# Kernel tuning notes

Hardware: AMD Instinct MI355X
Metric: run time of the kernel (lower is better)

Reference implementation:

```python
import jax, jax.numpy as jnp
import numpy as np

N_NODES = 50000


def _gcn_conv(x, edge_index, W, b):
    """PyG-style GCNConv: add self-loops, symmetric deg^-1/2 norm, linear + scatter-add + bias."""
    n = x.shape[0]
    # add self loops
    loop = jnp.arange(n, dtype=edge_index.dtype)
    src = jnp.concatenate([edge_index[0], loop])  # [E+N]
    dst = jnp.concatenate([edge_index[1], loop])
    ones = jnp.ones_like(dst, dtype=x.dtype)
    deg = jax.ops.segment_sum(ones, dst, num_segments=n)  # in-degree incl. self loop
    deg_inv_sqrt = jnp.where(deg > 0, jax.lax.rsqrt(deg), 0.0)
    norm = deg_inv_sqrt[src] * deg_inv_sqrt[dst]  # [E+N]
    h = x @ W  # [N, out]
    msg = h[src] * norm[:, None]  # gather + scale, [E+N, out]
    out = jax.ops.segment_sum(msg, dst, num_segments=n)  # scatter-add
    return out + b


def setup_inputs() -> dict:
    key = jax.random.key(0)
    k1, k2, k3, k4 = jax.random.split(key, 4)
    in_ch, hid, z = 128, 128, 64
    x = jax.random.normal(k1, (N_NODES, in_ch), dtype=jnp.float32)
    edge_index = jax.random.randint(k2, (2, 800000), 0, N_NODES, dtype=jnp.int64)
    W1 = jax.random.normal(k3, (in_ch, hid), dtype=jnp.float32) * (1.0 / np.sqrt(in_ch))
    b1 = jnp.zeros((hid,), dtype=jnp.float32)
    W2 = jax.random.normal(k4, (hid, z), dtype=jnp.float32) * (1.0 / np.sqrt(hid))
    b2 = jnp.zeros((z,), dtype=jnp.float32)
    return {"x": x, "edge_index": edge_index, "W1": W1, "b1": b1, "W2": W2, "b2": b2}


def reference(x, edge_index, W1, b1, W2, b2):
    h = jax.nn.relu(_gcn_conv(x, edge_index, W1, b1))
    return _gcn_conv(h, edge_index, W2, b2)
```

## Files before the change

kernel.cpp:

```cpp
#include <hip/hip_runtime.h>

static constexpr int K = 128;

using ushort8 = __attribute__((ext_vector_type(8))) unsigned short;
using bf16x8  = __attribute__((ext_vector_type(8))) __bf16;
using f32x4   = __attribute__((ext_vector_type(4))) float;

__device__ inline float bflo(unsigned u) { return __uint_as_float(u << 16); }
__device__ inline float bfhi(unsigned u) { return __uint_as_float(u & 0xFFFF0000u); }
__device__ inline unsigned short f2bf(float f) {
    unsigned u = __float_as_uint(f);
    return (unsigned short)((u + 0x7FFF + ((u >> 16) & 1)) >> 16);
}


__global__ __launch_bounds__(256) void k_zerob(int* __restrict__ bcnt) {
    bcnt[threadIdx.x] = 0;
}

__global__ __launch_bounds__(256) void k_bcount(const int* __restrict__ dst, int e,
                                                int* __restrict__ bcnt, int nb) {
    __shared__ int c[256];
    int t = threadIdx.x;
    c[t] = 0;
    __syncthreads();
    for (int i = blockIdx.x * 256 + t; i < e; i += gridDim.x * 256)
        atomicAdd(&c[dst[i] >> 8], 1);
    __syncthreads();
    if (t < nb && c[t]) atomicAdd(&bcnt[t], c[t]);
}

__global__ __launch_bounds__(256) void k_bscan(const int* __restrict__ bcnt,
                                               int* __restrict__ bbase,
                                               int* __restrict__ gcur,
                                               int nb, int* __restrict__ offs,
                                               int n, int e) {
    __shared__ int sh[256];
    int t = threadIdx.x;
    int v = (t < nb) ? bcnt[t] : 0;
    sh[t] = v;
    __syncthreads();
    for (int o = 1; o < 256; o <<= 1) {
        int x = (t >= o) ? sh[t - o] : 0;
        __syncthreads();
        sh[t] += x;
        __syncthreads();
    }
    int excl = sh[t] - v;
    bbase[t] = excl;
    gcur[t] = excl;
    if (t == 255) bbase[256] = sh[255];
    if (t == 0) offs[n] = e;
}

__global__ __launch_bounds__(256) void k_bin(const int* __restrict__ ei, int e,
                                             int* __restrict__ gcur,
                                             unsigned long long* __restrict__ tmp) {
    constexpr int PER = 8;
    __shared__ int cnt[256], base[256], cur[256];
    int t = threadIdx.x;
    int chunk0 = blockIdx.x * 256 * PER;
    cnt[t] = 0;
    __syncthreads();
    int ds[PER];
#pragma unroll
    for (int k2 = 0; k2 < PER; ++k2) {
        int i = chunk0 + k2 * 256 + t;
        ds[k2] = (i < e) ? ei[(size_t)e + i] : -1;
        if (ds[k2] >= 0) atomicAdd(&cnt[ds[k2] >> 8], 1);
    }
    __syncthreads();
    int c = cnt[t];
    base[t] = c ? atomicAdd(&gcur[t], c) : 0;
    cur[t] = 0;
    __syncthreads();
#pragma unroll
    for (int k2 = 0; k2 < PER; ++k2) {
        int i = chunk0 + k2 * 256 + t;
        if (i < e) {
            int b = ds[k2] >> 8;
            int pos = base[b] + atomicAdd(&cur[b], 1);
            tmp[pos] = ((unsigned long long)(unsigned)ds[k2] << 32) | (unsigned)ei[i];
        }
    }
}

__global__ __launch_bounds__(256) void k_csr(const unsigned long long* __restrict__ tmp,
                                             const int* __restrict__ bbase,
                                             int* __restrict__ offs,
                                             int* __restrict__ srt,
                                             float* __restrict__ dinv, int n) {
    __shared__ int cntS[256], sh[256], cur[256];
    int b = blockIdx.x;
    int t = threadIdx.x;
    int beg = bbase[b], end = bbase[b + 1];
    cntS[t] = 0;
    __syncthreads();
    for (int i = beg + t; i < end; i += 256)
        atomicAdd(&cntS[(int)(tmp[i] >> 32) & 255], 1);
    __syncthreads();
    int v = cntS[t];
    sh[t] = v;
    __syncthreads();
    for (int o = 1; o < 256; o <<= 1) {
        int x = (t >= o) ? sh[t - o] : 0;
        __syncthreads();
        sh[t] += x;
        __syncthreads();
    }
    int pfx = sh[t] - v;
    int node = b * 256 + t;
    if (node < n) {
        offs[node] = beg + pfx;
        dinv[node] = rsqrtf((float)(v + 1));
    }
    cur[t] = pfx;
    __syncthreads();
    for (int i = beg + t; i < end; i += 256) {
        unsigned long long pr = tmp[i];
        int d = (int)(pr >> 32);
        int pos = atomicAdd(&cur[d & 255], 1);
        srt[beg + pos] = (int)(pr & 0xFFFFFFFFu);
    }
}


template <int COUT>
__global__ __launch_bounds__(256) void k_gemm_mfma(const float* __restrict__ X,
                                                   const float* __restrict__ W,
                                                   const float* __restrict__ dinv,
                                                   unsigned short* __restrict__ G, int n) {
    constexpr int BM = 64, BK = 32;
    constexpr int NCT = COUT / 16;
    constexpr int NCH = K / BK;
    constexpr int WT = COUT * (BK / 8) / 256;
    __shared__ unsigned short Ah[BM * BK], Al[BM * BK];
    __shared__ unsigned short Bh[COUT * BK], Bl[COUT * BK];
    __shared__ float dS[BM];
    const int tid = threadIdx.x;
    const int row0 = blockIdx.x * BM;
    if (tid < BM) {
        int gr = row0 + tid;
        dS[tid] = (gr < n) ? dinv[gr] : 0.f;
    }

    float4 xr[2];
    float wr[WT][8];

    auto loadX = [&](int kc) {
        int r = tid >> 2, ks = tid & 3;
        int gr = row0 + r;
        if (gr < n) {
            const float4* pp = (const float4*)(X + (size_t)gr * K + kc * BK + ks * 8);
            xr[0] = pp[0];
            xr[1] = pp[1];
        } else {
            xr[0] = make_float4(0.f, 0.f, 0.f, 0.f);
            xr[1] = xr[0];
        }
    };
    auto loadW = [&](int kc) {
#pragma unroll
        for (int q = 0; q < WT; ++q) {
            int i = tid + q * 256;
            int c = i % COUT, ks = i / COUT;
#pragma unroll
            for (int j = 0; j < 8; ++j)
                wr[q][j] = W[(size_t)(kc * BK + ks * 8 + j) * COUT + c];
        }
    };
    auto storeLDS = [&]() {
        int r = tid >> 2, ks = tid & 3;
        ushort8 h, l;
        const float* f = (const float*)&xr[0];
#pragma unroll
        for (int j = 0; j < 8; ++j) {
            unsigned short hh = f2bf(f[j]);
            h[j] = hh;
            l[j] = f2bf(f[j] - __uint_as_float((unsigned)hh << 16));
        }
        *(ushort8*)&Ah[r * BK + ks * 8] = h;
        *(ushort8*)&Al[r * BK + ks * 8] = l;
#pragma unroll
        for (int q = 0; q < WT; ++q) {
            int i = tid + q * 256;
            int c = i % COUT, ks2 = i / COUT;
            ushort8 wh, wl;
#pragma unroll
            for (int j = 0; j < 8; ++j) {
                unsigned short hh = f2bf(wr[q][j]);
                wh[j] = hh;
                wl[j] = f2bf(wr[q][j] - __uint_as_float((unsigned)hh << 16));
            }
            *(ushort8*)&Bh[c * BK + ks2 * 8] = wh;
            *(ushort8*)&Bl[c * BK + ks2 * 8] = wl;
        }
    };

    f32x4 acc[NCT] = {};
    const int l = tid & 63, wv = tid >> 6;
    const int l16 = l & 15, lk = l >> 4;
    const int arow = wv * 16 + l16;

    loadX(0);
    loadW(0);
    storeLDS();
    __syncthreads();
    for (int c = 0; c < NCH; ++c) {
        if (c + 1 < NCH) { loadX(c + 1); loadW(c + 1); }
        bf16x8 ah = *(const bf16x8*)&Ah[arow * BK + lk * 8];
        bf16x8 al = *(const bf16x8*)&Al[arow * BK + lk * 8];
#pragma unroll
        for (int ct = 0; ct < NCT; ++ct) {
            bf16x8 bh = *(const bf16x8*)&Bh[(ct * 16 + l16) * BK + lk * 8];
            bf16x8 bl = *(const bf16x8*)&Bl[(ct * 16 + l16) * BK + lk * 8];
            acc[ct] = __builtin_amdgcn_mfma_f32_16x16x32_bf16(ah, bh, acc[ct], 0, 0, 0);
            acc[ct] = __builtin_amdgcn_mfma_f32_16x16x32_bf16(al, bh, acc[ct], 0, 0, 0);
            acc[ct] = __builtin_amdgcn_mfma_f32_16x16x32_bf16(ah, bl, acc[ct], 0, 0, 0);
        }
        if (c + 1 < NCH) {
            __syncthreads();
            storeLDS();
            __syncthreads();
        }
    }

#pragma unroll
    for (int ct = 0; ct < NCT; ++ct) {
        int col = ct * 16 + l16;
#pragma unroll
        for (int r4 = 0; r4 < 4; ++r4) {
            int lr = wv * 16 + lk * 4 + r4;
            int gr = row0 + lr;
            if (gr < n) G[(size_t)gr * COUT + col] = f2bf(acc[ct][r4] * dS[lr]);
        }
    }
}


#define ADD8(u)                                      \
    do {                                             \
        a[0] += bflo((u).x); a[1] += bfhi((u).x);    \
        a[2] += bflo((u).y); a[3] += bfhi((u).y);    \
        a[4] += bflo((u).z); a[5] += bfhi((u).z);    \
        a[6] += bflo((u).w); a[7] += bfhi((u).w);    \
    } while (0)

template <bool RELU>
__global__ __launch_bounds__(256) void k_reduce128(const int* __restrict__ offs,
                                                   const int* __restrict__ srt,
                                                   const uint4* __restrict__ g4,
                                                   const float* __restrict__ dinv,
                                                   const float* __restrict__ bias,
                                                   float* __restrict__ out, int n) {
    int node = blockIdx.x * 4 + (threadIdx.x >> 6);
    if (node >= n) return;
    int lane = threadIdx.x & 63;
    int l16 = lane & 15, grp = lane >> 4;
    int beg = offs[node], end = offs[node + 1];

    float a[8] = {};
    if (grp == 0) {
        uint4 u = g4[(size_t)node * 16 + l16];
        ADD8(u);
    }
    int j = beg + grp;
    for (; j + 12 < end; j += 16) {
        uint4 u0 = g4[(size_t)srt[j]      * 16 + l16];
        uint4 u1 = g4[(size_t)srt[j + 4]  * 16 + l16];
        uint4 u2 = g4[(size_t)srt[j + 8]  * 16 + l16];
        uint4 u3 = g4[(size_t)srt[j + 12] * 16 + l16];
        ADD8(u0); ADD8(u1); ADD8(u2); ADD8(u3);
    }
    for (; j < end; j += 4) {
        uint4 u = g4[(size_t)srt[j] * 16 + l16];
        ADD8(u);
    }
#pragma unroll
    for (int q = 0; q < 8; ++q) {
        a[q] += __shfl_xor(a[q], 16);
        a[q] += __shfl_xor(a[q], 32);
    }
    if (lane < 16) {
        float di = dinv[node];
        float4 b0 = ((const float4*)bias)[l16 * 2];
        float4 b1 = ((const float4*)bias)[l16 * 2 + 1];
        float4 o0, o1;
        o0.x = fmaf(di, a[0], b0.x); o0.y = fmaf(di, a[1], b0.y);
        o0.z = fmaf(di, a[2], b0.z); o0.w = fmaf(di, a[3], b0.w);
        o1.x = fmaf(di, a[4], b1.x); o1.y = fmaf(di, a[5], b1.y);
        o1.z = fmaf(di, a[6], b1.z); o1.w = fmaf(di, a[7], b1.w);
        if (RELU) {
            o0.x = fmaxf(o0.x, 0.f); o0.y = fmaxf(o0.y, 0.f);
            o0.z = fmaxf(o0.z, 0.f); o0.w = fmaxf(o0.w, 0.f);
            o1.x = fmaxf(o1.x, 0.f); o1.y = fmaxf(o1.y, 0.f);
            o1.z = fmaxf(o1.z, 0.f); o1.w = fmaxf(o1.w, 0.f);
        }
        float4* op = (float4*)(out + (size_t)node * 128 + l16 * 8);
        op[0] = o0;
        op[1] = o1;
    }
}

template <bool RELU>
__global__ __launch_bounds__(256) void k_reduce64(const int* __restrict__ offs,
                                                  const int* __restrict__ srt,
                                                  const uint4* __restrict__ g4,
                                                  const float* __restrict__ dinv,
                                                  const float* __restrict__ bias,
                                                  float* __restrict__ out, int n) {
    int node = blockIdx.x * 4 + (threadIdx.x >> 6);
    if (node >= n) return;
    int lane = threadIdx.x & 63;
    int l8 = lane & 7, grp = lane >> 3;
    int beg = offs[node], end = offs[node + 1];

    float a[8] = {};
    if (grp == 0) {
        uint4 u = g4[(size_t)node * 8 + l8];
        ADD8(u);
    }
    int j = beg + grp;
    for (; j + 8 < end; j += 16) {
        uint4 u0 = g4[(size_t)srt[j]     * 8 + l8];
        uint4 u1 = g4[(size_t)srt[j + 8] * 8 + l8];
        ADD8(u0); ADD8(u1);
    }
    for (; j < end; j += 8) {
        uint4 u = g4[(size_t)srt[j] * 8 + l8];
        ADD8(u);
    }
#pragma unroll
    for (int q = 0; q < 8; ++q) {
        a[q] += __shfl_xor(a[q], 8);
        a[q] += __shfl_xor(a[q], 16);
        a[q] += __shfl_xor(a[q], 32);
    }
    if (lane < 8) {
        float di = dinv[node];
        float4 b0 = ((const float4*)bias)[l8 * 2];
        float4 b1 = ((const float4*)bias)[l8 * 2 + 1];
        float4 o0, o1;
        o0.x = fmaf(di, a[0], b0.x); o0.y = fmaf(di, a[1], b0.y);
        o0.z = fmaf(di, a[2], b0.z); o0.w = fmaf(di, a[3], b0.w);
        o1.x = fmaf(di, a[4], b1.x); o1.y = fmaf(di, a[5], b1.y);
        o1.z = fmaf(di, a[6], b1.z); o1.w = fmaf(di, a[7], b1.w);
        if (RELU) {
            o0.x = fmaxf(o0.x, 0.f); o0.y = fmaxf(o0.y, 0.f);
            o0.z = fmaxf(o0.z, 0.f); o0.w = fmaxf(o0.w, 0.f);
            o1.x = fmaxf(o1.x, 0.f); o1.y = fmaxf(o1.y, 0.f);
            o1.z = fmaxf(o1.z, 0.f); o1.w = fmaxf(o1.w, 0.f);
        }
        float4* op = (float4*)(out + (size_t)node * 64 + l8 * 8);
        op[0] = o0;
        op[1] = o1;
    }
}

extern "C" void kernel_launch(void* const* d_in, const int* in_sizes, int n_in,
                              void* d_out, int out_size, void* d_ws, size_t ws_size,
                              hipStream_t stream) {
    const float* x  = (const float*)d_in[0];
    const int*   ei = (const int*)d_in[1];
    const float* W1 = (const float*)d_in[2];
    const float* b1 = (const float*)d_in[3];
    const float* W2 = (const float*)d_in[4];
    const float* b2 = (const float*)d_in[5];
    float* out = (float*)d_out;

    const int n = in_sizes[0] / K;
    const int e = in_sizes[1] / 2;
    const int nb = (n + 255) / 256;

    char* p = (char*)d_ws;
    unsigned long long* tmp = (unsigned long long*)p;  p += (size_t)e * 8;
    int* bcnt  = (int*)p;  p += 256 * 4;
    int* bbase = (int*)p;  p += 257 * 4;
    int* gcur  = (int*)p;  p += 256 * 4;
    int* offs  = (int*)p;  p += (size_t)(n + 1) * 4;
    int* srt   = (int*)p;  p += (size_t)e * 4;
    float* dinv = (float*)p;  p += (size_t)n * 4;
    p = (char*)(((uintptr_t)p + 15) & ~(uintptr_t)15);
    unsigned short* G1 = (unsigned short*)p;  p += (size_t)n * 128 * 2;
    p = (char*)(((uintptr_t)p + 15) & ~(uintptr_t)15);
    float* H = (float*)p;  p += (size_t)n * 128 * 4;
    p = (char*)(((uintptr_t)p + 15) & ~(uintptr_t)15);
    unsigned short* G2 = (unsigned short*)p;

    k_zerob<<<1, 256, 0, stream>>>(bcnt);
    k_bcount<<<512, 256, 0, stream>>>(ei + e, e, bcnt, nb);
    k_bscan<<<1, 256, 0, stream>>>(bcnt, bbase, gcur, nb, offs, n, e);
    k_bin<<<(e + 2047) / 2048, 256, 0, stream>>>(ei, e, gcur, tmp);
    k_csr<<<nb, 256, 0, stream>>>(tmp, bbase, offs, srt, dinv, n);

    k_gemm_mfma<128><<<(n + 63) / 64, 256, 0, stream>>>(x, W1, dinv, G1, n);
    k_reduce128<true><<<(n + 3) / 4, 256, 0, stream>>>(offs, srt, (const uint4*)G1,
                                                       dinv, b1, H, n);

    k_gemm_mfma<64><<<(n + 63) / 64, 256, 0, stream>>>(H, W2, dinv, G2, n);
    k_reduce64<false><<<(n + 3) / 4, 256, 0, stream>>>(offs, srt, (const uint4*)G2,
                                                       dinv, b2, out, n);
}
```

Before: 156.0 us.

## Split gather-reduce kernels across feature halves and retune CSR build launches

Both aggregation kernels now launch a second grid dimension that splits the feature columns in half. Each half-block handles narrower column slices with more edge-parallel lanes per node, which gives more parallelism per node and more loads in flight. The CSR build kernel moves to 1024-thread blocks and the binning kernel processes fewer edges per block. The zeroing kernel is replaced by hipMemsetAsync. The split doubles the neighbor-index reads and the number of blocks, and adds one more shuffle-reduction step per block.

```diff
diff --git a/kernel.cpp b/kernel.cpp
--- a/kernel.cpp
+++ b/kernel.cpp
@@ -13,10 +13,6 @@
     return (unsigned short)((u + 0x7FFF + ((u >> 16) & 1)) >> 16);
 }
 
-
-__global__ __launch_bounds__(256) void k_zerob(int* __restrict__ bcnt) {
-    bcnt[threadIdx.x] = 0;
-}
 
 __global__ __launch_bounds__(256) void k_bcount(const int* __restrict__ dst, int e,
                                                 int* __restrict__ bcnt, int nb) {
@@ -56,7 +52,7 @@
 __global__ __launch_bounds__(256) void k_bin(const int* __restrict__ ei, int e,
                                              int* __restrict__ gcur,
                                              unsigned long long* __restrict__ tmp) {
-    constexpr int PER = 8;
+    constexpr int PER = 4;
     __shared__ int cnt[256], base[256], cur[256];
     int t = threadIdx.x;
     int chunk0 = blockIdx.x * 256 * PER;
@@ -85,38 +81,40 @@
     }
 }
 
-__global__ __launch_bounds__(256) void k_csr(const unsigned long long* __restrict__ tmp,
-                                             const int* __restrict__ bbase,
-                                             int* __restrict__ offs,
-                                             int* __restrict__ srt,
-                                             float* __restrict__ dinv, int n) {
+__global__ __launch_bounds__(1024) void k_csr(const unsigned long long* __restrict__ tmp,
+                                              const int* __restrict__ bbase,
+                                              int* __restrict__ offs,
+                                              int* __restrict__ srt,
+                                              float* __restrict__ dinv, int n) {
     __shared__ int cntS[256], sh[256], cur[256];
     int b = blockIdx.x;
     int t = threadIdx.x;
     int beg = bbase[b], end = bbase[b + 1];
-    cntS[t] = 0;
-    __syncthreads();
-    for (int i = beg + t; i < end; i += 256)
+    if (t < 256) cntS[t] = 0;
+    __syncthreads();
+    for (int i = beg + t; i < end; i += 1024)
         atomicAdd(&cntS[(int)(tmp[i] >> 32) & 255], 1);
     __syncthreads();
-    int v = cntS[t];
-    sh[t] = v;
+    int v = (t < 256) ? cntS[t] : 0;
+    if (t < 256) sh[t] = v;
     __syncthreads();
     for (int o = 1; o < 256; o <<= 1) {
-        int x = (t >= o) ? sh[t - o] : 0;
+        int x = (t < 256 && t >= o) ? sh[t - o] : 0;
         __syncthreads();
-        sh[t] += x;
+        if (t < 256) sh[t] += x;
         __syncthreads();
     }
-    int pfx = sh[t] - v;
-    int node = b * 256 + t;
-    if (node < n) {
-        offs[node] = beg + pfx;
-        dinv[node] = rsqrtf((float)(v + 1));
-    }
-    cur[t] = pfx;
-    __syncthreads();
-    for (int i = beg + t; i < end; i += 256) {
+    if (t < 256) {
+        int pfx = sh[t] - v;
+        int node = b * 256 + t;
+        if (node < n) {
+            offs[node] = beg + pfx;
+            dinv[node] = rsqrtf((float)(v + 1));
+        }
+        cur[t] = pfx;
+    }
+    __syncthreads();
+    for (int i = beg + t; i < end; i += 1024) {
         unsigned long long pr = tmp[i];
         int d = (int)(pr >> 32);
         int pos = atomicAdd(&cur[d & 255], 1);
@@ -255,36 +253,37 @@
                                                    float* __restrict__ out, int n) {
     int node = blockIdx.x * 4 + (threadIdx.x >> 6);
     if (node >= n) return;
+    const int half = blockIdx.y;
     int lane = threadIdx.x & 63;
-    int l16 = lane & 15, grp = lane >> 4;
+    int l8 = lane & 7, grp = lane >> 3;
     int beg = offs[node], end = offs[node + 1];
+    const int cofs = half * 8 + l8;
 
     float a[8] = {};
     if (grp == 0) {
-        uint4 u = g4[(size_t)node * 16 + l16];
+        uint4 u = g4[(size_t)node * 16 + cofs];
         ADD8(u);
     }
     int j = beg + grp;
-    for (; j + 12 < end; j += 16) {
-        uint4 u0 = g4[(size_t)srt[j]      * 16 + l16];
-        uint4 u1 = g4[(size_t)srt[j + 4]  * 16 + l16];
-        uint4 u2 = g4[(size_t)srt[j + 8]  * 16 + l16];
-        uint4 u3 = g4[(size_t)srt[j + 12] * 16 + l16];
-        ADD8(u0); ADD8(u1); ADD8(u2); ADD8(u3);
-    }
-    for (; j < end; j += 4) {
-        uint4 u = g4[(size_t)srt[j] * 16 + l16];
+    for (; j + 8 < end; j += 16) {
+        uint4 u0 = g4[(size_t)srt[j]     * 16 + cofs];
+        uint4 u1 = g4[(size_t)srt[j + 8] * 16 + cofs];
+        ADD8(u0); ADD8(u1);
+    }
+    for (; j < end; j += 8) {
+        uint4 u = g4[(size_t)srt[j] * 16 + cofs];
         ADD8(u);
     }
 #pragma unroll
     for (int q = 0; q < 8; ++q) {
+        a[q] += __shfl_xor(a[q], 8);
         a[q] += __shfl_xor(a[q], 16);
         a[q] += __shfl_xor(a[q], 32);
     }
-    if (lane < 16) {
+    if (lane < 8) {
         float di = dinv[node];
-        float4 b0 = ((const float4*)bias)[l16 * 2];
-        float4 b1 = ((const float4*)bias)[l16 * 2 + 1];
+        float4 b0 = ((const float4*)bias)[half * 16 + l8 * 2];
+        float4 b1 = ((const float4*)bias)[half * 16 + l8 * 2 + 1];
         float4 o0, o1;
         o0.x = fmaf(di, a[0], b0.x); o0.y = fmaf(di, a[1], b0.y);
         o0.z = fmaf(di, a[2], b0.z); o0.w = fmaf(di, a[3], b0.w);
@@ -296,7 +295,7 @@
             o1.x = fmaxf(o1.x, 0.f); o1.y = fmaxf(o1.y, 0.f);
             o1.z = fmaxf(o1.z, 0.f); o1.w = fmaxf(o1.w, 0.f);
         }
-        float4* op = (float4*)(out + (size_t)node * 128 + l16 * 8);
+        float4* op = (float4*)(out + (size_t)node * 128 + half * 64 + l8 * 8);
         op[0] = o0;
         op[1] = o1;
     }
@@ -311,35 +310,38 @@
                                                   float* __restrict__ out, int n) {
     int node = blockIdx.x * 4 + (threadIdx.x >> 6);
     if (node >= n) return;
+    const int half = blockIdx.y;
     int lane = threadIdx.x & 63;
-    int l8 = lane & 7, grp = lane >> 3;
+    int l4 = lane & 3, grp = lane >> 2;
     int beg = offs[node], end = offs[node + 1];
+    const int cofs = half * 4 + l4;
 
     float a[8] = {};
     if (grp == 0) {
-        uint4 u = g4[(size_t)node * 8 + l8];
+        uint4 u = g4[(size_t)node * 8 + cofs];
         ADD8(u);
     }
     int j = beg + grp;
-    for (; j + 8 < end; j += 16) {
-        uint4 u0 = g4[(size_t)srt[j]     * 8 + l8];
-        uint4 u1 = g4[(size_t)srt[j + 8] * 8 + l8];
+    for (; j + 16 < end; j += 32) {
+        uint4 u0 = g4[(size_t)srt[j]      * 8 + cofs];
+        uint4 u1 = g4[(size_t)srt[j + 16] * 8 + cofs];
         ADD8(u0); ADD8(u1);
     }
-    for (; j < end; j += 8) {
-        uint4 u = g4[(size_t)srt[j] * 8 + l8];
+    for (; j < end; j += 16) {
+        uint4 u = g4[(size_t)srt[j] * 8 + cofs];
         ADD8(u);
     }
 #pragma unroll
     for (int q = 0; q < 8; ++q) {
+        a[q] += __shfl_xor(a[q], 4);
         a[q] += __shfl_xor(a[q], 8);
         a[q] += __shfl_xor(a[q], 16);
         a[q] += __shfl_xor(a[q], 32);
     }
-    if (lane < 8) {
+    if (lane < 4) {
         float di = dinv[node];
-        float4 b0 = ((const float4*)bias)[l8 * 2];
-        float4 b1 = ((const float4*)bias)[l8 * 2 + 1];
+        float4 b0 = ((const float4*)bias)[half * 8 + l4 * 2];
+        float4 b1 = ((const float4*)bias)[half * 8 + l4 * 2 + 1];
         float4 o0, o1;
         o0.x = fmaf(di, a[0], b0.x); o0.y = fmaf(di, a[1], b0.y);
         o0.z = fmaf(di, a[2], b0.z); o0.w = fmaf(di, a[3], b0.w);
@@ -351,7 +353,7 @@
             o1.x = fmaxf(o1.x, 0.f); o1.y = fmaxf(o1.y, 0.f);
             o1.z = fmaxf(o1.z, 0.f); o1.w = fmaxf(o1.w, 0.f);
         }
-        float4* op = (float4*)(out + (size_t)node * 64 + l8 * 8);
+        float4* op = (float4*)(out + (size_t)node * 64 + half * 32 + l4 * 8);
         op[0] = o0;
         op[1] = o1;
     }
@@ -387,17 +389,17 @@
     p = (char*)(((uintptr_t)p + 15) & ~(uintptr_t)15);
     unsigned short* G2 = (unsigned short*)p;
 
-    k_zerob<<<1, 256, 0, stream>>>(bcnt);
+    hipMemsetAsync(bcnt, 0, 256 * sizeof(int), stream);
     k_bcount<<<512, 256, 0, stream>>>(ei + e, e, bcnt, nb);
     k_bscan<<<1, 256, 0, stream>>>(bcnt, bbase, gcur, nb, offs, n, e);
-    k_bin<<<(e + 2047) / 2048, 256, 0, stream>>>(ei, e, gcur, tmp);
-    k_csr<<<nb, 256, 0, stream>>>(tmp, bbase, offs, srt, dinv, n);
+    k_bin<<<(e + 1023) / 1024, 256, 0, stream>>>(ei, e, gcur, tmp);
+    k_csr<<<nb, 1024, 0, stream>>>(tmp, bbase, offs, srt, dinv, n);
 
     k_gemm_mfma<128><<<(n + 63) / 64, 256, 0, stream>>>(x, W1, dinv, G1, n);
-    k_reduce128<true><<<(n + 3) / 4, 256, 0, stream>>>(offs, srt, (const uint4*)G1,
-                                                       dinv, b1, H, n);
+    k_reduce128<true><<<dim3((n + 3) / 4, 2), 256, 0, stream>>>(offs, srt, (const uint4*)G1,
+                                                                dinv, b1, H, n);
 
     k_gemm_mfma<64><<<(n + 63) / 64, 256, 0, stream>>>(H, W2, dinv, G2, n);
-    k_reduce64<false><<<(n + 3) / 4, 256, 0, stream>>>(offs, srt, (const uint4*)G2,
-                                                       dinv, b2, out, n);
-}
+    k_reduce64<false><<<dim3((n + 3) / 4, 2), 256, 0, stream>>>(offs, srt, (const uint4*)G2,
+                                                                dinv, b2, out, n);
+}
```

After: 192.7 us. +23.5%, slower.
